# Kernel tuning notes

Measured on AMD Instinct MI355X. Metric: run time of the kernel, lower is better.

The kernel has to match this reference:

```python
import jax, jax.numpy as jnp
import numpy as np

B, T, C, K, NH, HID, L, NC = 16, 500, 512, 7, 8, 2048, 3, 2
HD = C // NH
SCALE = float(1.0 / np.sqrt(HD))


def setup_inputs() -> dict:
    key = jax.random.key(0)
    ks = jax.random.split(key, 24)
    rn = lambda k, sh, s=0.02: jax.random.normal(k, sh, jnp.float32) * s
    return {
        'x': jax.random.normal(ks[0], (B, T, C), jnp.float32),
        'dw_w': rn(ks[1], (L, NC, C, 1, K)),   # depthwise conv kernels (groups=C)
        'dw_b': rn(ks[2], (L, NC, C)),
        'pw_w': rn(ks[3], (L, NC, C, C)),       # pointwise 1x1 conv weights [out,in]
        'pw_b': rn(ks[4], (L, NC, C)),
        'cln_g': jnp.ones((L, NC, C), jnp.float32),
        'cln_b': jnp.zeros((L, NC, C), jnp.float32),
        'wq': rn(ks[5], (L, C, C)), 'bq': rn(ks[6], (L, C)),
        'wk': rn(ks[7], (L, C, C)), 'bk': rn(ks[8], (L, C)),
        'wv': rn(ks[9], (L, C, C)), 'bv': rn(ks[10], (L, C)),
        'wo': rn(ks[11], (L, C, C)), 'bo': rn(ks[12], (L, C)),
        'aln_g': jnp.ones((L, C), jnp.float32), 'aln_b': jnp.zeros((L, C), jnp.float32),
        'w1': rn(ks[13], (L, HID, C)), 'b1': rn(ks[14], (L, HID)),
        'w2': rn(ks[15], (L, C, HID)), 'b2': rn(ks[16], (L, C)),
        'fln_g': jnp.ones((L, C), jnp.float32), 'fln_b': jnp.zeros((L, C), jnp.float32),
    }


def _ln(x, g, b):
    m = x.mean(-1, keepdims=True)
    v = ((x - m) ** 2).mean(-1, keepdims=True)
    return (x - m) / jnp.sqrt(v + 1e-5) * g + b


def _conv_block(x, w, b, pw, pb, g, be):
    # x: (B, C, T). Depthwise conv (groups=C), padding K//2 keeps T.
    out = jax.lax.conv_general_dilated(
        x, w, window_strides=(1,), padding=[(K // 2, K // 2)],
        feature_group_count=C, dimension_numbers=('NCH', 'OIH', 'NCH')) + b[None, :, None]
    out = jnp.einsum('bct,oc->bot', out, pw) + pb[None, :, None]  # pointwise 1x1
    out = _ln(out.transpose(0, 2, 1), g, be).transpose(0, 2, 1)
    return out


def _attn(x, wq, bq, wk, bk, wv, bv, wo, bo):
    Bx, Tx, Cx = x.shape
    def split(h):
        return h.reshape(Bx, Tx, NH, HD).transpose(0, 2, 1, 3)  # (B,H,T,HD)
    q = split(x @ wq.T + bq)
    k = split(x @ wk.T + bk)
    v = split(x @ wv.T + bv)
    att = jnp.einsum('bhqd,bhkd->bhqk', q, k) * SCALE
    mask = jnp.tril(jnp.ones((Tx, Tx), bool))
    att = jnp.where(mask, att, -1e10)
    att = jax.nn.softmax(att, axis=-1)
    y = jnp.einsum('bhqk,bhkd->bhqd', att, v)
    y = y.transpose(0, 2, 1, 3).reshape(Bx, Tx, Cx)
    return y @ wo.T + bo


def _block(x, l, dw_w, dw_b, pw_w, pw_b, cln_g, cln_b, wq, bq, wk, bk, wv, bv,
           wo, bo, aln_g, aln_b, w1, b1, w2, b2, fln_g, fln_b):
    out = x.transpose(0, 2, 1)  # (B, C, T)
    for c in range(NC):
        out = _conv_block(out, dw_w[l, c], dw_b[l, c], pw_w[l, c], pw_b[l, c],
                          cln_g[l, c], cln_b[l, c])
    out = out.transpose(0, 2, 1)  # (B, T, C)
    out = _attn(out, wq[l], bq[l], wk[l], bk[l], wv[l], bv[l], wo[l], bo[l])
    out = _ln(out, aln_g[l], aln_b[l])
    out = _ln(jax.nn.relu(out @ w1[l].T + b1[l]) @ w2[l].T + b2[l], fln_g[l], fln_b[l])
    return out  # eval mode: dropouts are identity


def reference(x, dw_w, dw_b, pw_w, pw_b, cln_g, cln_b, wq, bq, wk, bk, wv, bv,
              wo, bo, aln_g, aln_b, w1, b1, w2, b2, fln_g, fln_b):
    outs = []
    h = x
    for l in range(L):
        h = _block(h, l, dw_w, dw_b, pw_w, pw_b, cln_g, cln_b, wq, bq, wk, bk,
                   wv, bv, wo, bo, aln_g, aln_b, w1, b1, w2, b2, fln_g, fln_b)
        outs.append(h)
    return tuple(outs)
```

## Files before the change

kernel.cpp:

```cpp
#include <hip/hip_runtime.h>
#include <hip/hip_bf16.h>

namespace {
constexpr int B = 16, T = 500, C = 512, KW = 7, NH = 8, HD = 64, HID = 2048;
constexpr int M = B * T;
constexpr float SCALE = 0.125f;
constexpr int BTC = B * T * C;
constexpr int CC = C * C;
constexpr int SEG_PW0 = 0;
constexpr int SEG_PW1 = CC;
constexpr int SEG_WQ  = 2 * CC;
constexpr int SEG_WK  = 3 * CC;
constexpr int SEG_WV  = 4 * CC;
constexpr int SEG_WO  = 5 * CC;
constexpr int SEG_W1  = 6 * CC;
constexpr int SEG_W2  = 6 * CC + HID * C;
constexpr int SEG_END = 6 * CC + 2 * HID * C;
}

typedef short s16x8 __attribute__((ext_vector_type(8)));
typedef float f32x4v __attribute__((ext_vector_type(4)));

__device__ __forceinline__ unsigned int bfrne(float f) {
  unsigned int u = __float_as_uint(f);
  return (u + 0x7fffu + ((u >> 16) & 1u)) >> 16;
}
__device__ __forceinline__ unsigned int pack2(float a, float b) {
  return bfrne(a) | (bfrne(b) << 16);
}

__global__ __launch_bounds__(256) void cvtx_kernel(
    const float* __restrict__ X, unsigned short* __restrict__ Y) {
  size_t e = ((size_t)blockIdx.x * 256 + threadIdx.x) * 8;
  float4 a = *(const float4*)(X + e);
  float4 b = *(const float4*)(X + e + 4);
  uint4 o;
  o.x = pack2(a.x, a.y); o.y = pack2(a.z, a.w);
  o.z = pack2(b.x, b.y); o.w = pack2(b.z, b.w);
  *(uint4*)(Y + e) = o;
}

__global__ __launch_bounds__(256) void cvtw_kernel(
    const float* __restrict__ pw0, const float* __restrict__ pw1,
    const float* __restrict__ wqp, const float* __restrict__ wkp,
    const float* __restrict__ wvp, const float* __restrict__ wop,
    const float* __restrict__ w1p, const float* __restrict__ w2p,
    unsigned short* __restrict__ dst) {
  size_t e = ((size_t)blockIdx.x * 256 + threadIdx.x) * 8;
  const float* src;
  size_t off;
  if      (e < SEG_PW1) { src = pw0; off = e - SEG_PW0; }
  else if (e < SEG_WQ)  { src = pw1; off = e - SEG_PW1; }
  else if (e < SEG_WK)  { src = wqp; off = e - SEG_WQ; }
  else if (e < SEG_WV)  { src = wkp; off = e - SEG_WK; }
  else if (e < SEG_WO)  { src = wvp; off = e - SEG_WV; }
  else if (e < SEG_W1)  { src = wop; off = e - SEG_WO; }
  else if (e < SEG_W2)  { src = w1p; off = e - SEG_W1; }
  else                  { src = w2p; off = e - SEG_W2; }
  float4 a = *(const float4*)(src + off);
  float4 b = *(const float4*)(src + off + 4);
  uint4 o;
  o.x = pack2(a.x, a.y); o.y = pack2(a.z, a.w);
  o.z = pack2(b.x, b.y); o.w = pack2(b.z, b.w);
  *(uint4*)(dst + e) = o;
}

template <bool XBF, bool RELU, bool YBF>
__global__ __launch_bounds__(256) void gemm_mfma(
    const void* __restrict__ Xv, const unsigned short* __restrict__ Wb,
    const float* __restrict__ bias, void* __restrict__ Yv, int N, int K) {
  __shared__ unsigned short As[128 * 40];
  __shared__ unsigned short Bs[128 * 40];
  const int tid = threadIdx.x;
  const int n0 = blockIdx.x * 128, m0 = blockIdx.y * 128;
  const int w = tid >> 6, lane = tid & 63;
  const int mh = (w & 1) * 64, nh = (w >> 1) * 64;
  const int quad = lane >> 4, r15 = lane & 15;

  const int row0 = tid >> 2,           kq0 = (tid & 3) * 8;
  const int row1 = (tid + 256) >> 2,   kq1 = (tid & 3) * 8;
  const int xr0 = min(m0 + row0, M - 1), xr1 = min(m0 + row1, M - 1);
  const int wr0 = n0 + row0, wr1 = n0 + row1;

  f32x4v acc[4][4];
#pragma unroll
  for (int i = 0; i < 4; ++i)
#pragma unroll
    for (int j = 0; j < 4; ++j) acc[i][j] = {0.f, 0.f, 0.f, 0.f};

  auto loadX = [&](int k0, int xr, int kq) -> uint4 {
    if (XBF) {
      return *(const uint4*)((const unsigned short*)Xv + (size_t)xr * K + k0 + kq);
    } else {
      const float* xp = (const float*)Xv + (size_t)xr * K + k0 + kq;
      float4 a = *(const float4*)xp;
      float4 b = *(const float4*)(xp + 4);
      uint4 o;
      o.x = pack2(a.x, a.y); o.y = pack2(a.z, a.w);
      o.z = pack2(b.x, b.y); o.w = pack2(b.z, b.w);
      return o;
    }
  };
  auto loadW = [&](int k0, int wr, int kq) -> uint4 {
    return *(const uint4*)(Wb + (size_t)wr * K + k0 + kq);
  };

  uint4 xv0 = loadX(0, xr0, kq0), xv1 = loadX(0, xr1, kq1);
  uint4 wv0 = loadW(0, wr0, kq0), wv1 = loadW(0, wr1, kq1);
  const int nk = K / 32;
  for (int c = 0; c < nk; ++c) {
    __syncthreads();
    *(uint4*)&As[row0 * 40 + kq0] = xv0;
    *(uint4*)&As[row1 * 40 + kq1] = xv1;
    *(uint4*)&Bs[row0 * 40 + kq0] = wv0;
    *(uint4*)&Bs[row1 * 40 + kq1] = wv1;
    __syncthreads();
    if (c + 1 < nk) {
      int k0 = (c + 1) * 32;
      xv0 = loadX(k0, xr0, kq0); xv1 = loadX(k0, xr1, kq1);
      wv0 = loadW(k0, wr0, kq0); wv1 = loadW(k0, wr1, kq1);
    }
    s16x8 af[4], bg[4];
#pragma unroll
    for (int im = 0; im < 4; ++im)
      af[im] = *(const s16x8*)&As[(mh + im * 16 + r15) * 40 + quad * 8];
#pragma unroll
    for (int in = 0; in < 4; ++in)
      bg[in] = *(const s16x8*)&Bs[(nh + in * 16 + r15) * 40 + quad * 8];
#pragma unroll
    for (int in = 0; in < 4; ++in)
#pragma unroll
      for (int im = 0; im < 4; ++im)
        acc[im][in] = __builtin_amdgcn_mfma_f32_16x16x32_bf16(
            af[im], bg[in], acc[im][in], 0, 0, 0);
  }
#pragma unroll
  for (int in = 0; in < 4; ++in) {
    int col = n0 + nh + in * 16 + r15;
    float bv = bias[col];
#pragma unroll
    for (int im = 0; im < 4; ++im) {
      int rowb = m0 + mh + im * 16 + quad * 4;
#pragma unroll
      for (int r = 0; r < 4; ++r) {
        int row = rowb + r;
        if (row < M) {
          float v = acc[im][in][r] + bv;
          if (RELU) v = fmaxf(v, 0.f);
          if (YBF)
            ((unsigned short*)Yv)[(size_t)row * N + col] =
                (unsigned short)bfrne(v);
          else
            ((float*)Yv)[(size_t)row * N + col] = v;
        }
      }
    }
  }
}

__global__ __launch_bounds__(256) void dwconv_kernel(
    const float* __restrict__ X, const float* __restrict__ W,
    const float* __restrict__ bias, float* __restrict__ Y) {
  int gid = blockIdx.x * 256 + threadIdx.x;
  int b = blockIdx.y;
  int t = gid >> 9;
  int c = gid & 511;
  float acc = bias[c];
  size_t base = (size_t)b * T * C;
#pragma unroll
  for (int k = 0; k < KW; ++k) {
    int tt = t + k - 3;
    if (tt >= 0 && tt < T) acc += X[base + (size_t)tt * C + c] * W[c * KW + k];
  }
  Y[base + gid] = acc;
}

__global__ __launch_bounds__(256) void ln_kernel(
    const float* __restrict__ X, const float* __restrict__ g,
    const float* __restrict__ bta, float* __restrict__ Y) {
  int row = blockIdx.x * 4 + (threadIdx.x >> 6);
  int lane = threadIdx.x & 63;
  const float* x = X + (size_t)row * C;
  float v[8];
  float s = 0.f, ss = 0.f;
#pragma unroll
  for (int i = 0; i < 8; ++i) {
    v[i] = x[lane + i * 64];
    s += v[i];
    ss += v[i] * v[i];
  }
#pragma unroll
  for (int off = 32; off; off >>= 1) {
    s += __shfl_xor(s, off);
    ss += __shfl_xor(ss, off);
  }
  float mean = s * (1.f / C);
  float var = ss * (1.f / C) - mean * mean;
  var = fmaxf(var, 0.f);
  float rstd = rsqrtf(var + 1e-5f);
  float* y = Y + (size_t)row * C;
#pragma unroll
  for (int i = 0; i < 8; ++i) {
    int c = lane + i * 64;
    y[c] = (v[i] - mean) * rstd * g[c] + bta[c];
  }
}

__global__ __launch_bounds__(256) void attn_mfma_kernel(
    const float* __restrict__ Qg, const float* __restrict__ Kg,
    const float* __restrict__ Vg, float* __restrict__ Yg) {
  constexpr int LDK = 72;
  __shared__ __align__(16) unsigned short Ks[64 * LDK];
  __shared__ __align__(16) unsigned short Vt[64 * LDK];
  __shared__ __align__(16) unsigned short Ps[4][16 * LDK];
  const int tid = threadIdx.x;
  const int lane = tid & 63, w = tid >> 6;
  const int quad = lane >> 4, r15 = lane & 15;
  const int qt = blockIdx.x, hh = blockIdx.y, b = blockIdx.z;
  const int q0 = qt * 64;
  const size_t cbase = (size_t)hh * HD;
  const size_t bTC = (size_t)b * T * C;

  s16x8 qa[2];
  {
    int qr = min(q0 + w * 16 + r15, T - 1);
    const float* qp = Qg + bTC + (size_t)qr * C + cbase;
#pragma unroll
    for (int ks = 0; ks < 2; ++ks) {
      float4 a = *(const float4*)(qp + ks * 32 + quad * 8);
      float4 c = *(const float4*)(qp + ks * 32 + quad * 8 + 4);
      uint4 o;
      o.x = pack2(a.x * SCALE, a.y * SCALE);
      o.y = pack2(a.z * SCALE, a.w * SCALE);
      o.z = pack2(c.x * SCALE, c.y * SCALE);
      o.w = pack2(c.z * SCALE, c.w * SCALE);
      qa[ks] = *(s16x8*)&o;
    }
  }

  f32x4v oacc[4];
  float mm[4], ll[4];
#pragma unroll
  for (int i = 0; i < 4; ++i) {
    oacc[i] = {0.f, 0.f, 0.f, 0.f};
    mm[i] = -1e30f;
    ll[i] = 0.f;
  }

  const int krow = tid >> 2, kd = (tid & 3) * 4;
  const int vk4 = (tid >> 4) * 4, vd4 = (tid & 15) * 4;

  const int kend = min(q0 + 63, T - 1);
  for (int key0 = 0; key0 <= kend; key0 += 64) {
    __syncthreads();
    {
      int key = key0 + krow;
      if (key < T) {
        const float* kp = Kg + bTC + (size_t)key * C + cbase + kd;
#pragma unroll
        for (int u = 0; u < 4; ++u) {
          float4 kk = *(const float4*)(kp + u * 16);
          uint2 o2;
          o2.x = pack2(kk.x, kk.y);
          o2.y = pack2(kk.z, kk.w);
          *(uint2*)&Ks[krow * LDK + kd + u * 16] = o2;
        }
      } else {
        uint2 z;
        z.x = 0u; z.y = 0u;
#pragma unroll
        for (int u = 0; u < 4; ++u)
          *(uint2*)&Ks[krow * LDK + kd + u * 16] = z;
      }
    }
    {
      __align__(16) float va[4][4];
#pragma unroll
      for (int j = 0; j < 4; ++j) {
        int key = key0 + vk4 + j;
        if (key < T) {
          *(float4*)va[j] =
              *(const float4*)(Vg + bTC + (size_t)key * C + cbase + vd4);
        } else {
          va[j][0] = 0.f; va[j][1] = 0.f; va[j][2] = 0.f; va[j][3] = 0.f;
        }
      }
#pragma unroll
      for (int i = 0; i < 4; ++i) {
        uint2 o2;
        o2.x = pack2(va[0][i], va[1][i]);
        o2.y = pack2(va[2][i], va[3][i]);
        *(uint2*)&Vt[(vd4 + i) * LDK + vk4] = o2;
      }
    }
    __syncthreads();

    f32x4v sa[4];
#pragma unroll
    for (int nt = 0; nt < 4; ++nt) {
      s16x8 kb0 = *(const s16x8*)&Ks[(nt * 16 + r15) * LDK + quad * 8];
      s16x8 kb1 = *(const s16x8*)&Ks[(nt * 16 + r15) * LDK + 32 + quad * 8];
      f32x4v z = {0.f, 0.f, 0.f, 0.f};
      z = __builtin_amdgcn_mfma_f32_16x16x32_bf16(qa[0], kb0, z, 0, 0, 0);
      z = __builtin_amdgcn_mfma_f32_16x16x32_bf16(qa[1], kb1, z, 0, 0, 0);
      sa[nt] = z;
    }
    const bool diag = (key0 == q0);

#pragma unroll
    for (int r = 0; r < 4; ++r) {
      int q = q0 + w * 16 + quad * 4 + r;
      float sv[4];
#pragma unroll
      for (int nt = 0; nt < 4; ++nt) {
        sv[nt] = sa[nt][r];
        if (diag && (key0 + nt * 16 + r15 > q)) sv[nt] = -1e30f;
      }
      float mx = fmaxf(fmaxf(sv[0], sv[1]), fmaxf(sv[2], sv[3]));
      mx = fmaxf(mx, __shfl_xor(mx, 8));
      mx = fmaxf(mx, __shfl_xor(mx, 4));
      mx = fmaxf(mx, __shfl_xor(mx, 2));
      mx = fmaxf(mx, __shfl_xor(mx, 1));
      float mnew = fmaxf(mm[r], mx);
      float alpha = __expf(mm[r] - mnew);
      float ps = 0.f;
#pragma unroll
      for (int nt = 0; nt < 4; ++nt) {
        float p = __expf(sv[nt] - mnew);
        ps += p;
        Ps[w][(quad * 4 + r) * LDK + nt * 16 + r15] =
            (unsigned short)bfrne(p);
      }
      ps += __shfl_xor(ps, 8);
      ps += __shfl_xor(ps, 4);
      ps += __shfl_xor(ps, 2);
      ps += __shfl_xor(ps, 1);
      ll[r] = ll[r] * alpha + ps;
      mm[r] = mnew;
#pragma unroll
      for (int dt = 0; dt < 4; ++dt) oacc[dt][r] *= alpha;
    }
    asm volatile("s_waitcnt lgkmcnt(0)" ::: "memory");
    __builtin_amdgcn_sched_barrier(0);

    s16x8 pa0 = *(const s16x8*)&Ps[w][r15 * LDK + quad * 8];
    s16x8 pa1 = *(const s16x8*)&Ps[w][r15 * LDK + 32 + quad * 8];
#pragma unroll
    for (int dt = 0; dt < 4; ++dt) {
      s16x8 vb0 = *(const s16x8*)&Vt[(dt * 16 + r15) * LDK + quad * 8];
      s16x8 vb1 = *(const s16x8*)&Vt[(dt * 16 + r15) * LDK + 32 + quad * 8];
      oacc[dt] =
          __builtin_amdgcn_mfma_f32_16x16x32_bf16(pa0, vb0, oacc[dt], 0, 0, 0);
      oacc[dt] =
          __builtin_amdgcn_mfma_f32_16x16x32_bf16(pa1, vb1, oacc[dt], 0, 0, 0);
    }
  }

#pragma unroll
  for (int r = 0; r < 4; ++r) {
    int q = q0 + w * 16 + quad * 4 + r;
    if (q < T) {
      float inv = 1.f / ll[r];
      float* yp = Yg + bTC + (size_t)q * C + cbase;
#pragma unroll
      for (int dt = 0; dt < 4; ++dt) yp[dt * 16 + r15] = oacc[dt][r] * inv;
    }
  }
}

extern "C" void kernel_launch(void* const* d_in, const int* in_sizes, int n_in,
                              void* d_out, int out_size, void* d_ws,
                              size_t ws_size, hipStream_t stream) {
  const float* x     = (const float*)d_in[0];
  const float* dw_w  = (const float*)d_in[1];
  const float* dw_b  = (const float*)d_in[2];
  const float* pw_w  = (const float*)d_in[3];
  const float* pw_b  = (const float*)d_in[4];
  const float* cln_g = (const float*)d_in[5];
  const float* cln_b = (const float*)d_in[6];
  const float* wq    = (const float*)d_in[7];
  const float* bq    = (const float*)d_in[8];
  const float* wk    = (const float*)d_in[9];
  const float* bk    = (const float*)d_in[10];
  const float* wv    = (const float*)d_in[11];
  const float* bv    = (const float*)d_in[12];
  const float* wo    = (const float*)d_in[13];
  const float* bo    = (const float*)d_in[14];
  const float* aln_g = (const float*)d_in[15];
  const float* aln_b = (const float*)d_in[16];
  const float* w1    = (const float*)d_in[17];
  const float* b1    = (const float*)d_in[18];
  const float* w2    = (const float*)d_in[19];
  const float* b2    = (const float*)d_in[20];
  const float* fln_g = (const float*)d_in[21];
  const float* fln_b = (const float*)d_in[22];

  float* ws = (float*)d_ws;
  float* A  = ws;
  float* Bf = ws + (size_t)BTC;
  float* R0 = ws + (size_t)2 * BTC;
  float* R1 = ws + (size_t)3 * BTC;
  float* R2 = ws + (size_t)4 * BTC;
  unsigned short* WA = (unsigned short*)(ws + (size_t)5 * BTC);
  float* out = (float*)d_out;

  unsigned short* xbf  = (unsigned short*)Bf;
  unsigned short* fbf  = (unsigned short*)R1;
  unsigned short* hbf  = (unsigned short*)A;

  dim3 blk(256);
  dim3 gemmC(C / 128, 63);
  dim3 gemmH(HID / 128, 63);
  dim3 convG(T * C / 256, B);
  dim3 attnG((T + 63) / 64, NH, B);
  int cvtxB = BTC / 2048;
  int cvtwB = SEG_END / 2048;

  for (int l = 0; l < 3; ++l) {
    float* h = out + (size_t)l * BTC;
    const float* hin = (l == 0) ? x : out + (size_t)(l - 1) * BTC;
    cvtw_kernel<<<cvtwB, blk, 0, stream>>>(
        pw_w + (size_t)(2 * l) * CC, pw_w + (size_t)(2 * l + 1) * CC,
        wq + (size_t)l * CC, wk + (size_t)l * CC, wv + (size_t)l * CC,
        wo + (size_t)l * CC, w1 + (size_t)l * HID * C,
        w2 + (size_t)l * C * HID, WA);
    for (int cb = 0; cb < 2; ++cb) {
      int lc = l * 2 + cb;
      const float* src = (cb == 0) ? hin : h;
      dwconv_kernel<<<convG, blk, 0, stream>>>(src, dw_w + (size_t)lc * C * KW,
                                               dw_b + (size_t)lc * C, A);
      cvtx_kernel<<<cvtxB, blk, 0, stream>>>(A, xbf);
      gemm_mfma<true, false, false><<<gemmC, blk, 0, stream>>>(
          xbf, WA + (cb ? SEG_PW1 : SEG_PW0), pw_b + (size_t)lc * C, R0, C, C);
      ln_kernel<<<M / 4, blk, 0, stream>>>(R0, cln_g + (size_t)lc * C,
                                           cln_b + (size_t)lc * C, h);
    }
    cvtx_kernel<<<cvtxB, blk, 0, stream>>>(h, xbf);
    gemm_mfma<true, false, false><<<gemmC, blk, 0, stream>>>(
        xbf, WA + SEG_WQ, bq + (size_t)l * C, R0, C, C);
    gemm_mfma<true, false, false><<<gemmC, blk, 0, stream>>>(
        xbf, WA + SEG_WK, bk + (size_t)l * C, R1, C, C);
    gemm_mfma<true, false, false><<<gemmC, blk, 0, stream>>>(
        xbf, WA + SEG_WV, bv + (size_t)l * C, R2, C, C);
    attn_mfma_kernel<<<attnG, blk, 0, stream>>>(R0, R1, R2, A);
    cvtx_kernel<<<cvtxB, blk, 0, stream>>>(A, xbf);
    gemm_mfma<true, false, false><<<gemmC, blk, 0, stream>>>(
        xbf, WA + SEG_WO, bo + (size_t)l * C, R0, C, C);
    ln_kernel<<<M / 4, blk, 0, stream>>>(R0, aln_g + (size_t)l * C,
                                         aln_b + (size_t)l * C, h);
    cvtx_kernel<<<cvtxB, blk, 0, stream>>>(h, fbf);
    gemm_mfma<true, true, true><<<gemmH, blk, 0, stream>>>(
        fbf, WA + SEG_W1, b1 + (size_t)l * HID, hbf, HID, C);
    gemm_mfma<true, false, false><<<gemmC, blk, 0, stream>>>(
        hbf, WA + SEG_W2, b2 + (size_t)l * C, R0, C, HID);
    ln_kernel<<<M / 4, blk, 0, stream>>>(R0, fln_g + (size_t)l * C,
                                         fln_b + (size_t)l * C, h);
  }
}
```

Baseline: 1.216 ms.

## Fuse bf16 conversions into producers, merge QKV GEMM, double-buffer GEMM LDS

Removes the standalone fp32-to-bf16 conversion kernels. The depthwise conv, layernorm (dual fp32+bf16 output) and attention now write bf16 directly. The Q/K/V projections become one GEMM with N=1536 into an interleaved bf16 buffer, which attention reads directly, and the softmax scale is applied to scores instead of Q. The GEMM gains double-buffered LDS to drop one barrier per k-step. The layernorm and conv loads are vectorised. These changes cut memory traffic and kernel launches, but Q/K/V are now rounded to bf16 at the GEMM output and shared memory use doubles.

After: 1.067 ms. -12.3%, faster.

```diff
diff --git a/kernel.cpp b/kernel.cpp
--- a/kernel.cpp
+++ b/kernel.cpp
@@ -20,6 +20,7 @@
 
 typedef short s16x8 __attribute__((ext_vector_type(8)));
 typedef float f32x4v __attribute__((ext_vector_type(4)));
+typedef unsigned short u16x4 __attribute__((ext_vector_type(4)));
 
 __device__ __forceinline__ unsigned int bfrne(float f) {
   unsigned int u = __float_as_uint(f);
@@ -27,17 +28,6 @@
 }
 __device__ __forceinline__ unsigned int pack2(float a, float b) {
   return bfrne(a) | (bfrne(b) << 16);
-}
-
-__global__ __launch_bounds__(256) void cvtx_kernel(
-    const float* __restrict__ X, unsigned short* __restrict__ Y) {
-  size_t e = ((size_t)blockIdx.x * 256 + threadIdx.x) * 8;
-  float4 a = *(const float4*)(X + e);
-  float4 b = *(const float4*)(X + e + 4);
-  uint4 o;
-  o.x = pack2(a.x, a.y); o.y = pack2(a.z, a.w);
-  o.z = pack2(b.x, b.y); o.w = pack2(b.z, b.w);
-  *(uint4*)(Y + e) = o;
 }
 
 __global__ __launch_bounds__(256) void cvtw_kernel(
@@ -65,12 +55,20 @@
   *(uint4*)(dst + e) = o;
 }
 
+__global__ __launch_bounds__(256) void biascat_kernel(
+    const float* __restrict__ bq, const float* __restrict__ bk,
+    const float* __restrict__ bv, float* __restrict__ dst) {
+  int i = blockIdx.x * 256 + threadIdx.x;
+  float v = (i < 512) ? bq[i] : (i < 1024 ? bk[i - 512] : bv[i - 1024]);
+  dst[i] = v;
+}
+
 template <bool XBF, bool RELU, bool YBF>
 __global__ __launch_bounds__(256) void gemm_mfma(
     const void* __restrict__ Xv, const unsigned short* __restrict__ Wb,
     const float* __restrict__ bias, void* __restrict__ Yv, int N, int K) {
-  __shared__ unsigned short As[128 * 40];
-  __shared__ unsigned short Bs[128 * 40];
+  __shared__ unsigned short As[2][128 * 40];
+  __shared__ unsigned short Bs[2][128 * 40];
   const int tid = threadIdx.x;
   const int n0 = blockIdx.x * 128, m0 = blockIdx.y * 128;
   const int w = tid >> 6, lane = tid & 63;
@@ -107,32 +105,42 @@
 
   uint4 xv0 = loadX(0, xr0, kq0), xv1 = loadX(0, xr1, kq1);
   uint4 wv0 = loadW(0, wr0, kq0), wv1 = loadW(0, wr1, kq1);
+  *(uint4*)&As[0][row0 * 40 + kq0] = xv0;
+  *(uint4*)&As[0][row1 * 40 + kq1] = xv1;
+  *(uint4*)&Bs[0][row0 * 40 + kq0] = wv0;
+  *(uint4*)&Bs[0][row1 * 40 + kq1] = wv1;
+  int cur = 0;
   const int nk = K / 32;
   for (int c = 0; c < nk; ++c) {
-    __syncthreads();
-    *(uint4*)&As[row0 * 40 + kq0] = xv0;
-    *(uint4*)&As[row1 * 40 + kq1] = xv1;
-    *(uint4*)&Bs[row0 * 40 + kq0] = wv0;
-    *(uint4*)&Bs[row1 * 40 + kq1] = wv1;
     __syncthreads();
     if (c + 1 < nk) {
       int k0 = (c + 1) * 32;
       xv0 = loadX(k0, xr0, kq0); xv1 = loadX(k0, xr1, kq1);
       wv0 = loadW(k0, wr0, kq0); wv1 = loadW(k0, wr1, kq1);
     }
+    const unsigned short* Ac = As[cur];
+    const unsigned short* Bc = Bs[cur];
     s16x8 af[4], bg[4];
 #pragma unroll
     for (int im = 0; im < 4; ++im)
-      af[im] = *(const s16x8*)&As[(mh + im * 16 + r15) * 40 + quad * 8];
+      af[im] = *(const s16x8*)&Ac[(mh + im * 16 + r15) * 40 + quad * 8];
 #pragma unroll
     for (int in = 0; in < 4; ++in)
-      bg[in] = *(const s16x8*)&Bs[(nh + in * 16 + r15) * 40 + quad * 8];
+      bg[in] = *(const s16x8*)&Bc[(nh + in * 16 + r15) * 40 + quad * 8];
 #pragma unroll
     for (int in = 0; in < 4; ++in)
 #pragma unroll
       for (int im = 0; im < 4; ++im)
         acc[im][in] = __builtin_amdgcn_mfma_f32_16x16x32_bf16(
             af[im], bg[in], acc[im][in], 0, 0, 0);
+    if (c + 1 < nk) {
+      int nx = cur ^ 1;
+      *(uint4*)&As[nx][row0 * 40 + kq0] = xv0;
+      *(uint4*)&As[nx][row1 * 40 + kq1] = xv1;
+      *(uint4*)&Bs[nx][row0 * 40 + kq0] = wv0;
+      *(uint4*)&Bs[nx][row1 * 40 + kq1] = wv1;
+      cur = nx;
+    }
   }
 #pragma unroll
   for (int in = 0; in < 4; ++in) {
@@ -160,32 +168,40 @@
 
 __global__ __launch_bounds__(256) void dwconv_kernel(
     const float* __restrict__ X, const float* __restrict__ W,
-    const float* __restrict__ bias, float* __restrict__ Y) {
+    const float* __restrict__ bias, unsigned short* __restrict__ Y) {
   int gid = blockIdx.x * 256 + threadIdx.x;
   int b = blockIdx.y;
-  int t = gid >> 9;
-  int c = gid & 511;
-  float acc = bias[c];
+  int e = gid * 2;
+  int t = e >> 9;
+  int c = e & 511;
+  float acc0 = bias[c], acc1 = bias[c + 1];
   size_t base = (size_t)b * T * C;
 #pragma unroll
   for (int k = 0; k < KW; ++k) {
     int tt = t + k - 3;
-    if (tt >= 0 && tt < T) acc += X[base + (size_t)tt * C + c] * W[c * KW + k];
-  }
-  Y[base + gid] = acc;
-}
-
+    if (tt >= 0 && tt < T) {
+      float2 xv = *(const float2*)&X[base + (size_t)tt * C + c];
+      acc0 += xv.x * W[c * KW + k];
+      acc1 += xv.y * W[(c + 1) * KW + k];
+    }
+  }
+  *(unsigned int*)&Y[base + e] = pack2(acc0, acc1);
+}
+
+template <bool DUAL>
 __global__ __launch_bounds__(256) void ln_kernel(
     const float* __restrict__ X, const float* __restrict__ g,
-    const float* __restrict__ bta, float* __restrict__ Y) {
+    const float* __restrict__ bta, float* __restrict__ Y,
+    unsigned short* __restrict__ Yb) {
   int row = blockIdx.x * 4 + (threadIdx.x >> 6);
   int lane = threadIdx.x & 63;
-  const float* x = X + (size_t)row * C;
-  float v[8];
+  const float* x = X + (size_t)row * C + lane * 8;
+  float4 a = *(const float4*)x;
+  float4 b2 = *(const float4*)(x + 4);
+  float v[8] = {a.x, a.y, a.z, a.w, b2.x, b2.y, b2.z, b2.w};
   float s = 0.f, ss = 0.f;
 #pragma unroll
   for (int i = 0; i < 8; ++i) {
-    v[i] = x[lane + i * 64];
     s += v[i];
     ss += v[i] * v[i];
   }
@@ -198,17 +214,31 @@
   float var = ss * (1.f / C) - mean * mean;
   var = fmaxf(var, 0.f);
   float rstd = rsqrtf(var + 1e-5f);
-  float* y = Y + (size_t)row * C;
-#pragma unroll
-  for (int i = 0; i < 8; ++i) {
-    int c = lane + i * 64;
-    y[c] = (v[i] - mean) * rstd * g[c] + bta[c];
+  float4 g0 = *(const float4*)(g + lane * 8);
+  float4 g1 = *(const float4*)(g + lane * 8 + 4);
+  float4 be0 = *(const float4*)(bta + lane * 8);
+  float4 be1 = *(const float4*)(bta + lane * 8 + 4);
+  float gg[8] = {g0.x, g0.y, g0.z, g0.w, g1.x, g1.y, g1.z, g1.w};
+  float bb[8] = {be0.x, be0.y, be0.z, be0.w, be1.x, be1.y, be1.z, be1.w};
+  float o[8];
+#pragma unroll
+  for (int i = 0; i < 8; ++i) o[i] = (v[i] - mean) * rstd * gg[i] + bb[i];
+  float* y = Y + (size_t)row * C + lane * 8;
+  float4 w0 = {o[0], o[1], o[2], o[3]};
+  float4 w1 = {o[4], o[5], o[6], o[7]};
+  *(float4*)y = w0;
+  *(float4*)(y + 4) = w1;
+  if (DUAL) {
+    uint4 ob;
+    ob.x = pack2(o[0], o[1]); ob.y = pack2(o[2], o[3]);
+    ob.z = pack2(o[4], o[5]); ob.w = pack2(o[6], o[7]);
+    *(uint4*)(Yb + (size_t)row * C + lane * 8) = ob;
   }
 }
 
 __global__ __launch_bounds__(256) void attn_mfma_kernel(
-    const float* __restrict__ Qg, const float* __restrict__ Kg,
-    const float* __restrict__ Vg, float* __restrict__ Yg) {
+    const unsigned short* __restrict__ QKV, unsigned short* __restrict__ Yb) {
+  constexpr int QS = 3 * C;
   constexpr int LDK = 72;
   __shared__ __align__(16) unsigned short Ks[64 * LDK];
   __shared__ __align__(16) unsigned short Vt[64 * LDK];
@@ -218,24 +248,15 @@
   const int quad = lane >> 4, r15 = lane & 15;
   const int qt = blockIdx.x, hh = blockIdx.y, b = blockIdx.z;
   const int q0 = qt * 64;
-  const size_t cbase = (size_t)hh * HD;
-  const size_t bTC = (size_t)b * T * C;
+  const size_t hbase = (size_t)hh * HD;
 
   s16x8 qa[2];
   {
     int qr = min(q0 + w * 16 + r15, T - 1);
-    const float* qp = Qg + bTC + (size_t)qr * C + cbase;
-#pragma unroll
-    for (int ks = 0; ks < 2; ++ks) {
-      float4 a = *(const float4*)(qp + ks * 32 + quad * 8);
-      float4 c = *(const float4*)(qp + ks * 32 + quad * 8 + 4);
-      uint4 o;
-      o.x = pack2(a.x * SCALE, a.y * SCALE);
-      o.y = pack2(a.z * SCALE, a.w * SCALE);
-      o.z = pack2(c.x * SCALE, c.y * SCALE);
-      o.w = pack2(c.z * SCALE, c.w * SCALE);
-      qa[ks] = *(s16x8*)&o;
-    }
+    const unsigned short* qp = QKV + ((size_t)b * T + qr) * QS + hbase;
+#pragma unroll
+    for (int ks = 0; ks < 2; ++ks)
+      qa[ks] = *(const s16x8*)(qp + ks * 32 + quad * 8);
   }
 
   f32x4v oacc[4];
@@ -247,7 +268,7 @@
     ll[i] = 0.f;
   }
 
-  const int krow = tid >> 2, kd = (tid & 3) * 4;
+  const int krow = tid >> 2, kd = (tid & 3) * 16;
   const int vk4 = (tid >> 4) * 4, vd4 = (tid & 15) * 4;
 
   const int kend = min(q0 + 63, T - 1);
@@ -256,40 +277,35 @@
     {
       int key = key0 + krow;
       if (key < T) {
-        const float* kp = Kg + bTC + (size_t)key * C + cbase + kd;
-#pragma unroll
-        for (int u = 0; u < 4; ++u) {
-          float4 kk = *(const float4*)(kp + u * 16);
-          uint2 o2;
-          o2.x = pack2(kk.x, kk.y);
-          o2.y = pack2(kk.z, kk.w);
-          *(uint2*)&Ks[krow * LDK + kd + u * 16] = o2;
-        }
+        const unsigned short* kp =
+            QKV + ((size_t)b * T + key) * QS + C + hbase + kd;
+        uint4 k0 = *(const uint4*)kp;
+        uint4 k1 = *(const uint4*)(kp + 8);
+        *(uint4*)&Ks[krow * LDK + kd] = k0;
+        *(uint4*)&Ks[krow * LDK + kd + 8] = k1;
       } else {
-        uint2 z;
-        z.x = 0u; z.y = 0u;
-#pragma unroll
-        for (int u = 0; u < 4; ++u)
-          *(uint2*)&Ks[krow * LDK + kd + u * 16] = z;
+        uint4 z = {0u, 0u, 0u, 0u};
+        *(uint4*)&Ks[krow * LDK + kd] = z;
+        *(uint4*)&Ks[krow * LDK + kd + 8] = z;
       }
     }
     {
-      __align__(16) float va[4][4];
+      u16x4 va[4];
 #pragma unroll
       for (int j = 0; j < 4; ++j) {
         int key = key0 + vk4 + j;
         if (key < T) {
-          *(float4*)va[j] =
-              *(const float4*)(Vg + bTC + (size_t)key * C + cbase + vd4);
+          va[j] = *(const u16x4*)(QKV + ((size_t)b * T + key) * QS + 2 * C +
+                                  hbase + vd4);
         } else {
-          va[j][0] = 0.f; va[j][1] = 0.f; va[j][2] = 0.f; va[j][3] = 0.f;
+          va[j] = (u16x4){0, 0, 0, 0};
         }
       }
 #pragma unroll
       for (int i = 0; i < 4; ++i) {
         uint2 o2;
-        o2.x = pack2(va[0][i], va[1][i]);
-        o2.y = pack2(va[2][i], va[3][i]);
+        o2.x = (unsigned int)va[0][i] | ((unsigned int)va[1][i] << 16);
+        o2.y = (unsigned int)va[2][i] | ((unsigned int)va[3][i] << 16);
         *(uint2*)&Vt[(vd4 + i) * LDK + vk4] = o2;
       }
     }
@@ -313,7 +329,7 @@
       float sv[4];
 #pragma unroll
       for (int nt = 0; nt < 4; ++nt) {
-        sv[nt] = sa[nt][r];
+        sv[nt] = sa[nt][r] * SCALE;
         if (diag && (key0 + nt * 16 + r15 > q)) sv[nt] = -1e30f;
       }
       float mx = fmaxf(fmaxf(sv[0], sv[1]), fmaxf(sv[2], sv[3]));
@@ -361,9 +377,10 @@
     int q = q0 + w * 16 + quad * 4 + r;
     if (q < T) {
       float inv = 1.f / ll[r];
-      float* yp = Yg + bTC + (size_t)q * C + cbase;
-#pragma unroll
-      for (int dt = 0; dt < 4; ++dt) yp[dt * 16 + r15] = oacc[dt][r] * inv;
+      unsigned short* yp = Yb + ((size_t)b * T + q) * C + hbase;
+#pragma unroll
+      for (int dt = 0; dt < 4; ++dt)
+        yp[dt * 16 + r15] = (unsigned short)bfrne(oacc[dt][r] * inv);
     }
   }
 }
@@ -404,16 +421,18 @@
   unsigned short* WA = (unsigned short*)(ws + (size_t)5 * BTC);
   float* out = (float*)d_out;
 
-  unsigned short* xbf  = (unsigned short*)Bf;
-  unsigned short* fbf  = (unsigned short*)R1;
-  unsigned short* hbf  = (unsigned short*)A;
+  unsigned short* xbf   = (unsigned short*)Bf;
+  unsigned short* qkvbf = (unsigned short*)R0;
+  unsigned short* fbf   = (unsigned short*)R2;
+  unsigned short* hbf   = (unsigned short*)A;
+  float* qkvb = A;
 
   dim3 blk(256);
   dim3 gemmC(C / 128, 63);
+  dim3 gemmQKV(3 * C / 128, 63);
   dim3 gemmH(HID / 128, 63);
-  dim3 convG(T * C / 256, B);
+  dim3 convG(T * C / 512, B);
   dim3 attnG((T + 63) / 64, NH, B);
-  int cvtxB = BTC / 2048;
   int cvtwB = SEG_END / 2048;
 
   for (int l = 0; l < 3; ++l) {
@@ -424,36 +443,35 @@
         wq + (size_t)l * CC, wk + (size_t)l * CC, wv + (size_t)l * CC,
         wo + (size_t)l * CC, w1 + (size_t)l * HID * C,
         w2 + (size_t)l * C * HID, WA);
+    biascat_kernel<<<6, blk, 0, stream>>>(bq + (size_t)l * C,
+                                          bk + (size_t)l * C,
+                                          bv + (size_t)l * C, qkvb);
     for (int cb = 0; cb < 2; ++cb) {
       int lc = l * 2 + cb;
       const float* src = (cb == 0) ? hin : h;
       dwconv_kernel<<<convG, blk, 0, stream>>>(src, dw_w + (size_t)lc * C * KW,
-                                               dw_b + (size_t)lc * C, A);
-      cvtx_kernel<<<cvtxB, blk, 0, stream>>>(A, xbf);
+                                               dw_b + (size_t)lc * C, xbf);
       gemm_mfma<true, false, false><<<gemmC, blk, 0, stream>>>(
           xbf, WA + (cb ? SEG_PW1 : SEG_PW0), pw_b + (size_t)lc * C, R0, C, C);
-      ln_kernel<<<M / 4, blk, 0, stream>>>(R0, cln_g + (size_t)lc * C,
-                                           cln_b + (size_t)lc * C, h);
-    }
-    cvtx_kernel<<<cvtxB, blk, 0, stream>>>(h, xbf);
+      if (cb == 0)
+        ln_kernel<false><<<M / 4, blk, 0, stream>>>(
+            R0, cln_g + (size_t)lc * C, cln_b + (size_t)lc * C, h, nullptr);
+      else
+        ln_kernel<true><<<M / 4, blk, 0, stream>>>(
+            R0, cln_g + (size_t)lc * C, cln_b + (size_t)lc * C, h, xbf);
+    }
+    gemm_mfma<true, false, true><<<gemmQKV, blk, 0, stream>>>(
+        xbf, WA + SEG_WQ, qkvb, qkvbf, 3 * C, C);
+    attn_mfma_kernel<<<attnG, blk, 0, stream>>>(qkvbf, xbf);
     gemm_mfma<true, false, false><<<gemmC, blk, 0, stream>>>(
-        xbf, WA + SEG_WQ, bq + (size_t)l * C, R0, C, C);
-    gemm_mfma<true, false, false><<<gemmC, blk, 0, stream>>>(
-        xbf, WA + SEG_WK, bk + (size_t)l * C, R1, C, C);
-    gemm_mfma<true, false, false><<<gemmC, blk, 0, stream>>>(
-        xbf, WA + SEG_WV, bv + (size_t)l * C, R2, C, C);
-    attn_mfma_kernel<<<attnG, blk, 0, stream>>>(R0, R1, R2, A);
-    cvtx_kernel<<<cvtxB, blk, 0, stream>>>(A, xbf);
-    gemm_mfma<true, false, false><<<gemmC, blk, 0, stream>>>(
-        xbf, WA + SEG_WO, bo + (size_t)l * C, R0, C, C);
-    ln_kernel<<<M / 4, blk, 0, stream>>>(R0, aln_g + (size_t)l * C,
-                                         aln_b + (size_t)l * C, h);
-    cvtx_kernel<<<cvtxB, blk, 0, stream>>>(h, fbf);
+        xbf, WA + SEG_WO, bo + (size_t)l * C, R1, C, C);
+    ln_kernel<true><<<M / 4, blk, 0, stream>>>(
+        R1, aln_g + (size_t)l * C, aln_b + (size_t)l * C, h, fbf);
     gemm_mfma<true, true, true><<<gemmH, blk, 0, stream>>>(
         fbf, WA + SEG_W1, b1 + (size_t)l * HID, hbf, HID, C);
     gemm_mfma<true, false, false><<<gemmC, blk, 0, stream>>>(
         hbf, WA + SEG_W2, b2 + (size_t)l * C, R0, C, HID);
-    ln_kernel<<<M / 4, blk, 0, stream>>>(R0, fln_g + (size_t)l * C,
-                                         fln_b + (size_t)l * C, h);
-  }
-}
+    ln_kernel<false><<<M / 4, blk, 0, stream>>>(
+        R0, fln_g + (size_t)l * C, fln_b + (size_t)l * C, h, nullptr);
+  }
+}
```
